# Optimization experiments

Measured on AMD Instinct MI355X. Metric: run time of the kernel, lower is better.

## Reference

```python
import jax, jax.numpy as jnp
import numpy as np
from functools import partial

EPS = 1e-5
CHANS = [(3, 64), (64, 64), (64, 128), (128, 128), (128, 256), (256, 256), (256, 256), (256, 256)]

def conv3d(x, w):
    # x: [B,X,Y,Z,Cin], w: [3,3,3,Cin,Cout]; Minkowski stride-1 conv keeps coords -> SAME padding
    return jax.lax.conv_general_dilated(x, w, window_strides=(1, 1, 1), padding='SAME',
                                        dimension_numbers=('NDHWC', 'DHWIO', 'NDHWC'))

def bn(x, g, b):
    # training-mode batch norm over all voxels (MinkowskiBatchNorm forward)
    m = jnp.mean(x, axis=(0, 1, 2, 3))
    v = jnp.var(x, axis=(0, 1, 2, 3))
    return (x - m) * jax.lax.rsqrt(v + EPS) * g + b

def maxpool2(x):
    return jax.lax.reduce_window(x, -jnp.inf, jax.lax.max,
                                 (1, 2, 2, 2, 1), (1, 2, 2, 2, 1), 'VALID')

def setup_inputs() -> dict:
    key = jax.random.key(0)
    ks = jax.random.split(key, 32)
    inp = {'x': jax.random.normal(ks[0], (2, 64, 64, 64, 3), dtype=jnp.float32)}
    for i, (ci, co) in enumerate(CHANS):
        scale = (2.0 / (27 * ci)) ** 0.5  # kaiming for 3x3x3 conv
        inp[f'w{i+1}'] = jax.random.normal(ks[1 + i], (3, 3, 3, ci, co), dtype=jnp.float32) * scale
        inp[f'g{i+1}'] = jnp.ones((co,), dtype=jnp.float32)
        inp[f'b{i+1}'] = jnp.zeros((co,), dtype=jnp.float32)
    inp['wl'] = jax.random.normal(ks[20], (256, 256), dtype=jnp.float32) * (1.0 / 16.0)
    inp['bl'] = jnp.zeros((256,), dtype=jnp.float32)
    return inp

def reference(x, w1, g1, b1, w2, g2, b2, w3, g3, b3, w4, g4, b4,
              w5, g5, b5, w6, g6, b6, w7, g7, b7, w8, g8, b8, wl, bl):
    h = jax.nn.relu(bn(conv3d(x, w1), g1, b1))
    h = jax.nn.relu(bn(conv3d(h, w2), g2, b2))
    h = maxpool2(h)                                   # 64 -> 32
    h = jax.nn.relu(bn(conv3d(h, w3), g3, b3))
    h = jax.nn.relu(bn(conv3d(h, w4), g4, b4))
    h = maxpool2(h)                                   # 32 -> 16
    h = jax.nn.relu(bn(conv3d(h, w5), g5, b5))
    h = jax.nn.relu(bn(conv3d(h, w6), g6, b6))
    h = jax.nn.relu(bn(conv3d(h, w7), g7, b7))
    h = maxpool2(h)                                   # 16 -> 8
    h = bn(conv3d(h, w8), g8, b8)                     # no ReLU before global pool in source
    h = jnp.mean(h, axis=(1, 2, 3))                   # MinkowskiGlobalPooling (avg over coords)
    return h @ wl + bl                                # MinkowskiLinear(256, out_feat)
```

## Files before the change

### kernel.cpp

```cpp
#include <hip/hip_runtime.h>
#include <stdint.h>


typedef _Float16 f16;
typedef _Float16 f16x8 __attribute__((ext_vector_type(8)));
typedef _Float16 f16x4 __attribute__((ext_vector_type(4)));
typedef float f32x4 __attribute__((ext_vector_type(4)));

__device__ __forceinline__ int xcd_swz(int bx, int nbx) {
  const int q = nbx >> 3, r = nbx & 7;
  const int x = bx & 7, o = bx >> 3;
  return (x < r ? x * (q + 1) : r * (q + 1) + (x - r) * q) + o;
}

struct WArgs {
  const float* src[8];
  int end[8];
  int S[8], G[8], CR[8], CO[8];
};
__global__ __launch_bounds__(256) void wprep_all(WArgs a, f16* __restrict__ wf)
{
  const int e = blockIdx.x * 256 + threadIdx.x;
  int li = 0;
  while (li < 7 && e >= a.end[li]) ++li;
  if (e >= a.end[li]) return;
  const int base = li ? a.end[li - 1] : 0;
  int x = e - base;
  const int i = x & 7;
  const int l = (x >> 3) & 63;
  int r = x >> 9;
  const int g = r % a.G[li]; r /= a.G[li];
  const int s = r % a.S[li]; r /= a.S[li];
  const int t = r;
  const int k = s * 32 + ((l >> 4) << 3) + i;
  const int co = g * 16 + (l & 15);
  float v;
  if (li == 0) {
    const int tap = k >> 3, ci = k & 7;
    v = (ci < 3 && tap < 27) ? a.src[0][((long)tap * 3 + ci) * 64 + co] : 0.f;
  } else {
    v = (k < a.CR[li]) ? a.src[li][((long)t * a.CR[li] + k) * a.CO[li] + co] : 0.f;
  }
  wf[e] = (f16)v;
}

__global__ __launch_bounds__(256) void conv1_mfma(
    const float* __restrict__ xin, const f16* __restrict__ wf,
    f16* __restrict__ out, float* __restrict__ part)
{
  constexpr int Z = 64, Y = 64, X = 64, L = 4;
  constexpr int RB = 48;
  constexpr int SLAB = (L + 2) * (Z + 2) * RB;
  __shared__ __align__(16) char slab[3 * SLAB];
  __shared__ float sstat[4][2][64];

  const int tid = threadIdx.x;
  const int lane = tid & 63;
  const int wr = tid >> 6;

  const int bxs = xcd_swz(blockIdx.x, gridDim.x);
  const long vb = (long)bxs * 256;
  const int n = (int)(vb >> 18);
  const int rem = (int)(vb & 262143);
  const int x0 = rem >> 12;
  const int y0 = (rem >> 6) & 63;

  if (tid < 36) {
    const int s = tid / 12, pr = tid % 12;
    const int row = (pr >> 1) * (Z + 2) + (pr & 1) * (Z + 1);
    const f16x8 hz = {};
    *(f16x8*)(slab + s * SLAB + row * RB) = hz;
  }

  for (int rr2 = tid; rr2 < 3 * (L + 2) * Z; rr2 += 256) {
    const int s = rr2 / ((L + 2) * Z);
    const int rr = rr2 % ((L + 2) * Z);
    const int li = rr / Z, z = rr % Z;
    const int xs = x0 + s - 1, ys = y0 - 1 + li;
    f16x8 h = {};
    if (xs >= 0 && xs < X && ys >= 0 && ys < Y) {
      const float* p = xin + (((long)(n * X + xs) * Y + ys) * Z + z) * 3;
      h[0] = (f16)p[0]; h[1] = (f16)p[1]; h[2] = (f16)p[2];
    }
    *(f16x8*)(slab + s * SLAB + (li * (Z + 2) + 1 + z) * RB) = h;
  }

  int abase[4];
  #pragma unroll
  for (int r = 0; r < 4; ++r) {
    const int vl = wr * 64 + r * 16 + (lane & 15);
    abase[r] = ((vl >> 6) * (Z + 2) + (vl & 63)) * RB;
  }
  const int c = lane >> 4;
  int rofftab[7];
  #pragma unroll
  for (int j = 0; j < 7; ++j) {
    const int tap = 4 * j + c;
    if (tap < 27) {
      const int dx = tap / 9, dy = (tap / 3) % 3, dz = tap % 3;
      rofftab[j] = dx * SLAB + (dy * (Z + 2) + dz) * RB;
    } else {
      rofftab[j] = 0;
    }
  }

  f32x4 acc[4][4];
  const f32x4 fz = {0.f, 0.f, 0.f, 0.f};
  #pragma unroll
  for (int r = 0; r < 4; ++r)
    #pragma unroll
    for (int cc = 0; cc < 4; ++cc) acc[r][cc] = fz;

  __syncthreads();

  #pragma unroll
  for (int j = 0; j < 7; ++j) {
    f16x8 av[4];
    #pragma unroll
    for (int r = 0; r < 4; ++r)
      av[r] = *(const f16x8*)(slab + abase[r] + rofftab[j]);
    f16x8 bv[4];
    #pragma unroll
    for (int c2 = 0; c2 < 4; ++c2)
      bv[c2] = *(const f16x8*)((const char*)wf + ((j * 4 + c2) << 10) + (lane << 4));
    #pragma unroll
    for (int r = 0; r < 4; ++r)
      #pragma unroll
      for (int c2 = 0; c2 < 4; ++c2)
        acc[r][c2] = __builtin_amdgcn_mfma_f32_16x16x32_f16(av[r], bv[c2], acc[r][c2], 0, 0, 0);
  }

  const long vgbase = vb + wr * 64;
  #pragma unroll
  for (int r = 0; r < 4; ++r)
    #pragma unroll
    for (int cc = 0; cc < 4; ++cc)
      #pragma unroll
      for (int q = 0; q < 4; ++q) {
        const long vox = vgbase + r * 16 + ((lane >> 4) << 2) + q;
        const int co = cc * 16 + (lane & 15);
        out[vox * 64 + co] = (f16)acc[r][cc][q];
      }

  float s4[4], q4[4];
  #pragma unroll
  for (int cc = 0; cc < 4; ++cc) {
    float s = 0.f, q = 0.f;
    #pragma unroll
    for (int r = 0; r < 4; ++r)
      #pragma unroll
      for (int qd = 0; qd < 4; ++qd) {
        const float v = acc[r][cc][qd];
        s += v;
        q = fmaf(v, v, q);
      }
    s4[cc] = s; q4[cc] = q;
  }
  #pragma unroll
  for (int cc = 0; cc < 4; ++cc) {
    s4[cc] += __shfl_xor(s4[cc], 16);
    s4[cc] += __shfl_xor(s4[cc], 32);
    q4[cc] += __shfl_xor(q4[cc], 16);
    q4[cc] += __shfl_xor(q4[cc], 32);
  }
  if (lane < 16) {
    #pragma unroll
    for (int cc = 0; cc < 4; ++cc) {
      sstat[wr][0][cc * 16 + lane] = s4[cc];
      sstat[wr][1][cc * 16 + lane] = q4[cc];
    }
  }
  __syncthreads();
  for (int t = tid; t < 128; t += 256) {
    const int k = (t >> 6) & 1, ch = t & 63;
    float v = 0.f;
    #pragma unroll
    for (int w2 = 0; w2 < 4; ++w2) v += sstat[w2][k][ch];
    part[(long)bxs * 128 + k * 64 + ch] = v;
  }
}

__global__ __launch_bounds__(256) void bnpad(
    const f16* __restrict__ in, f16* __restrict__ outp,
    const float* __restrict__ sc, const float* __restrict__ sh)
{
  const long NT = 2L * 66 * 66 * 66 * 8;
  long idx = (long)blockIdx.x * 256 + threadIdx.x;
  if (idx >= NT) return;
  const int c8 = (int)(idx & 7);
  long v = idx >> 3;
  const int zp = (int)(v % 66); v /= 66;
  const int yp = (int)(v % 66); v /= 66;
  const int xp = (int)(v % 66);
  const int n = (int)(v / 66);
  f16x8 h = {};
  if (xp >= 1 && xp <= 64 && yp >= 1 && yp <= 64 && zp >= 1 && zp <= 64) {
    const long src = ((((long)n * 64 + xp - 1) * 64 + yp - 1) * 64 + zp - 1) * 64 + c8 * 8;
    h = *(const f16x8*)(in + src);
    const int ci = c8 * 8;
    const float4 s0 = *(const float4*)(sc + ci);
    const float4 s1 = *(const float4*)(sc + ci + 4);
    const float4 h0 = *(const float4*)(sh + ci);
    const float4 h1 = *(const float4*)(sh + ci + 4);
    h[0] = (f16)fmaxf(fmaf((float)h[0], s0.x, h0.x), 0.f);
    h[1] = (f16)fmaxf(fmaf((float)h[1], s0.y, h0.y), 0.f);
    h[2] = (f16)fmaxf(fmaf((float)h[2], s0.z, h0.z), 0.f);
    h[3] = (f16)fmaxf(fmaf((float)h[3], s0.w, h0.w), 0.f);
    h[4] = (f16)fmaxf(fmaf((float)h[4], s1.x, h1.x), 0.f);
    h[5] = (f16)fmaxf(fmaf((float)h[5], s1.y, h1.y), 0.f);
    h[6] = (f16)fmaxf(fmaf((float)h[6], s1.z, h1.z), 0.f);
    h[7] = (f16)fmaxf(fmaf((float)h[7], s1.w, h1.w), 0.f);
  }
  *(f16x8*)(outp + idx * 8) = h;
}

__global__ __launch_bounds__(256) void conv2_dma(
    const f16* __restrict__ xp, const f16* __restrict__ wf,
    f16* __restrict__ out, float* __restrict__ part)
{
  constexpr int ZP = 66;
  constexpr int RB = 128;
  constexpr int SLABB = 51200;
  __shared__ __align__(1024) char slab[SLABB];
  __shared__ float sstat[4][2][64];

  const int tid = threadIdx.x;
  const int lane = tid & 63;
  const int wv = tid >> 6;

  const int bxs = xcd_swz(blockIdx.x, gridDim.x);
  const long vb = (long)bxs * 256;
  const int n = (int)(vb >> 18);
  const int rem = (int)(vb & 262143);
  const int x0 = rem >> 12;
  const int y0 = (rem >> 6) & 63;

  const int srcoff = ((lane >> 3) << 7) | ((((lane & 7) ^ ((lane >> 3) & 7))) << 4);

  int arow[4];
  #pragma unroll
  for (int r = 0; r < 4; ++r) {
    const int vl = wv * 64 + r * 16 + (lane & 15);
    arow[r] = (vl >> 6) * ZP + (vl & 63);
  }
  const int kbyte = (lane >> 4) << 4;

  f32x4 acc[4][4];
  const f32x4 fz = {0.f, 0.f, 0.f, 0.f};
  #pragma unroll
  for (int r = 0; r < 4; ++r)
    #pragma unroll
    for (int c = 0; c < 4; ++c) acc[r][c] = fz;

  for (int dx = 0; dx < 3; ++dx) {
    __syncthreads();
    const char* gsrc = (const char*)xp +
        (((long)(n * 66 + (x0 + dx)) * 66 + y0) * (long)(ZP * 64 * 2));
    for (int i = wv; i < 50; i += 4) {
      __builtin_amdgcn_global_load_lds(
          (const __attribute__((address_space(1))) uint32_t*)(const void*)(gsrc + (long)i * 1024 + srcoff),
          (__attribute__((address_space(3))) uint32_t*)(void*)(slab + i * 1024),
          16, 0, 0);
    }
    __syncthreads();

    for (int s = 0; s < 2; ++s) {
      #pragma unroll
      for (int dy = 0; dy < 3; ++dy) {
        #pragma unroll
        for (int dzi = 0; dzi < 3; ++dzi) {
          f16x8 av[4];
          #pragma unroll
          for (int r = 0; r < 4; ++r) {
            const int row = arow[r] + dy * ZP + dzi;
            av[r] = *(const f16x8*)(slab + row * RB +
                      ((s * 64 + kbyte) ^ ((row & 7) << 4)));
          }
          const int t = dx * 9 + dy * 3 + dzi;
          f16x8 bv[4];
          #pragma unroll
          for (int c = 0; c < 4; ++c)
            bv[c] = *(const f16x8*)((const char*)wf +
                      (((long)(t * 2 + s) * 4 + c) << 10) + (lane << 4));
          #pragma unroll
          for (int r = 0; r < 4; ++r)
            #pragma unroll
            for (int c = 0; c < 4; ++c)
              acc[r][c] = __builtin_amdgcn_mfma_f32_16x16x32_f16(av[r], bv[c], acc[r][c], 0, 0, 0);
        }
      }
    }
  }

  const long vgbase = vb + wv * 64;
  #pragma unroll
  for (int r = 0; r < 4; ++r)
    #pragma unroll
    for (int c = 0; c < 4; ++c)
      #pragma unroll
      for (int q = 0; q < 4; ++q) {
        const long vox = vgbase + r * 16 + ((lane >> 4) << 2) + q;
        const int co = c * 16 + (lane & 15);
        out[vox * 64 + co] = (f16)acc[r][c][q];
      }

  float s4[4], q4[4];
  #pragma unroll
  for (int c = 0; c < 4; ++c) {
    float s = 0.f, q = 0.f;
    #pragma unroll
    for (int r = 0; r < 4; ++r)
      #pragma unroll
      for (int qd = 0; qd < 4; ++qd) {
        const float v = acc[r][c][qd];
        s += v;
        q = fmaf(v, v, q);
      }
    s4[c] = s; q4[c] = q;
  }
  #pragma unroll
  for (int c = 0; c < 4; ++c) {
    s4[c] += __shfl_xor(s4[c], 16);
    s4[c] += __shfl_xor(s4[c], 32);
    q4[c] += __shfl_xor(q4[c], 16);
    q4[c] += __shfl_xor(q4[c], 32);
  }
  if (lane < 16) {
    #pragma unroll
    for (int c = 0; c < 4; ++c) {
      sstat[wv][0][c * 16 + lane] = s4[c];
      sstat[wv][1][c * 16 + lane] = q4[c];
    }
  }
  __syncthreads();
  for (int t = tid; t < 128; t += 256) {
    const int k = (t >> 6) & 1, ch = t & 63;
    float v = 0.f;
    #pragma unroll
    for (int w2 = 0; w2 < 4; ++w2) v += sstat[w2][k][ch];
    part[(long)bxs * 128 + k * 64 + ch] = v;
  }
}

template<int CIN, int Z, int WR, int WC, bool HASBN, int SS>
__global__ __launch_bounds__(WR*WC*64) void conv_mfma(
    const f16* __restrict__ xin, const f16* __restrict__ wf,
    f16* __restrict__ out, int X, int Y, int Co,
    const float* __restrict__ sc, const float* __restrict__ sh,
    float* __restrict__ part, int partBase,
    float* __restrict__ pout, long outE)
{
  constexpr int NTHR = WR * WC * 64;
  constexpr int L = 64 * WR / Z;
  constexpr int RB = (CIN + 8) * 2;
  constexpr int S = CIN / 32;
  constexpr int COW = 64 * WC;
  constexpr bool SPLIT = (SS > 0);
  __shared__ __align__(16) char slab[(L + 2) * (Z + 2) * RB];
  __shared__ float sstat[SPLIT ? 1 : WR * WC][2][64];

  const int tid = threadIdx.x;
  const int lane = tid & 63;
  const int wv = tid >> 6;
  const int wr = wv / WC, wc = wv % WC;

  const int bxs = xcd_swz(blockIdx.x, gridDim.x);
  const long vb = (long)bxs * (64 * WR);
  const int XYZ = X * Y * Z;
  const int n = (int)(vb / XYZ);
  const int rem = (int)(vb % XYZ);
  const int x0 = rem / (Y * Z);
  const int y0 = (rem % (Y * Z)) / Z;
  const int co0 = blockIdx.y * COW;
  const int Gtot = Co >> 4;
  const int g0 = (co0 >> 4) + wc * 4;

  int abase[4];
  #pragma unroll
  for (int r = 0; r < 4; ++r) {
    const int vl = wr * 64 + r * 16 + (lane & 15);
    abase[r] = ((vl / Z) * (Z + 2) + (vl % Z)) * RB + ((lane >> 4) << 4);
  }

  f32x4 acc[4][4];
  const f32x4 fz = {0.f, 0.f, 0.f, 0.f};
  #pragma unroll
  for (int r = 0; r < 4; ++r)
    #pragma unroll
    for (int c = 0; c < 4; ++c) acc[r][c] = fz;

  {
    const f16x8 hz = {};
    for (int e = tid * 8; e < (L + 2) * 2 * CIN; e += NTHR * 8) {
      const int pr = e / CIN, ci = e % CIN;
      const int row = (pr >> 1) * (Z + 2) + (pr & 1) * (Z + 1);
      *(f16x8*)(slab + row * RB + ci * 2) = hz;
    }
  }

  auto stage = [&](int dx) {
    const int xs = x0 + dx - 1;
    const bool xok = (xs >= 0) && (xs < X);
    const long gv0 = ((long)(n * X + xs) * Y + (y0 - 1)) * Z;
    constexpr int NE = (L + 2) * Z * CIN;
    for (int e = tid * 8; e < NE; e += NTHR * 8) {
      const int rr = e / CIN, ci = e % CIN;
      const int li = rr / Z, z = rr % Z;
      const int ys = y0 - 1 + li;
      f16x8 h = {};
      if (xok && ys >= 0 && ys < Y) {
        h = *(const f16x8*)(xin + (gv0 + rr) * CIN + ci);
        if constexpr (HASBN) {
          const float4 s0 = *(const float4*)(sc + ci);
          const float4 s1 = *(const float4*)(sc + ci + 4);
          const float4 h0 = *(const float4*)(sh + ci);
          const float4 h1 = *(const float4*)(sh + ci + 4);
          h[0] = (f16)fmaxf(fmaf((float)h[0], s0.x, h0.x), 0.f);
          h[1] = (f16)fmaxf(fmaf((float)h[1], s0.y, h0.y), 0.f);
          h[2] = (f16)fmaxf(fmaf((float)h[2], s0.z, h0.z), 0.f);
          h[3] = (f16)fmaxf(fmaf((float)h[3], s0.w, h0.w), 0.f);
          h[4] = (f16)fmaxf(fmaf((float)h[4], s1.x, h1.x), 0.f);
          h[5] = (f16)fmaxf(fmaf((float)h[5], s1.y, h1.y), 0.f);
          h[6] = (f16)fmaxf(fmaf((float)h[6], s1.z, h1.z), 0.f);
          h[7] = (f16)fmaxf(fmaf((float)h[7], s1.w, h1.w), 0.f);
        }
      }
      *(f16x8*)(slab + (li * (Z + 2) + 1 + z) * RB + ci * 2) = h;
    }
  };

  auto ktaps = [&](int dx, int s) {
    #pragma unroll
    for (int dy = 0; dy < 3; ++dy) {
      #pragma unroll
      for (int dzi = 0; dzi < 3; ++dzi) {
        f16x8 av[4];
        #pragma unroll
        for (int r = 0; r < 4; ++r)
          av[r] = *(const f16x8*)(slab + abase[r] + s * 64 + (dy * (Z + 2) + dzi) * RB);
        const int t = dx * 9 + dy * 3 + dzi;
        f16x8 bv[4];
        #pragma unroll
        for (int c = 0; c < 4; ++c)
          bv[c] = *(const f16x8*)((const char*)wf +
                    (((long)(t * S + s) * Gtot + g0 + c) << 10) + (lane << 4));
        #pragma unroll
        for (int r = 0; r < 4; ++r)
          #pragma unroll
          for (int c = 0; c < 4; ++c)
            acc[r][c] = __builtin_amdgcn_mfma_f32_16x16x32_f16(av[r], bv[c], acc[r][c], 0, 0, 0);
      }
    }
  };

  if constexpr (SPLIT) {
    constexpr int SCH = S / SS;
    const int zb = blockIdx.z;
    const int dx = zb / SS;
    const int s0 = (zb % SS) * SCH;
    stage(dx);
    __syncthreads();
    #pragma unroll
    for (int si = 0; si < SCH; ++si) ktaps(dx, s0 + si);
  } else {
    for (int dx = 0; dx < 3; ++dx) {
      __syncthreads();
      stage(dx);
      __syncthreads();
      for (int s = 0; s < S; ++s) ktaps(dx, s);
    }
  }

  const long vgbase = vb + wr * 64;
  const int cobase = co0 + wc * 64;
  if constexpr (SPLIT) {
    float* pb = pout + (long)blockIdx.z * outE;
    #pragma unroll
    for (int r = 0; r < 4; ++r)
      #pragma unroll
      for (int c = 0; c < 4; ++c)
        #pragma unroll
        for (int q = 0; q < 4; ++q) {
          const long vox = vgbase + r * 16 + ((lane >> 4) << 2) + q;
          const int co = cobase + c * 16 + (lane & 15);
          pb[vox * Co + co] = acc[r][c][q];
        }
    return;
  }

  #pragma unroll
  for (int r = 0; r < 4; ++r)
    #pragma unroll
    for (int c = 0; c < 4; ++c)
      #pragma unroll
      for (int q = 0; q < 4; ++q) {
        const long vox = vgbase + r * 16 + ((lane >> 4) << 2) + q;
        const int co = cobase + c * 16 + (lane & 15);
        out[vox * Co + co] = (f16)acc[r][c][q];
      }

  float s4[4], q4[4];
  #pragma unroll
  for (int c = 0; c < 4; ++c) {
    float s = 0.f, q = 0.f;
    #pragma unroll
    for (int r = 0; r < 4; ++r)
      #pragma unroll
      for (int qd = 0; qd < 4; ++qd) {
        const float v = acc[r][c][qd];
        s += v;
        q = fmaf(v, v, q);
      }
    s4[c] = s; q4[c] = q;
  }
  #pragma unroll
  for (int c = 0; c < 4; ++c) {
    s4[c] += __shfl_xor(s4[c], 16);
    s4[c] += __shfl_xor(s4[c], 32);
    q4[c] += __shfl_xor(q4[c], 16);
    q4[c] += __shfl_xor(q4[c], 32);
  }
  if (lane < 16) {
    #pragma unroll
    for (int c = 0; c < 4; ++c) {
      sstat[wv][0][c * 16 + lane] = s4[c];
      sstat[wv][1][c * 16 + lane] = q4[c];
    }
  }
  __syncthreads();
  const long entry = (long)blockIdx.y * gridDim.x + bxs + partBase;
  for (int t = tid; t < WC * 128; t += NTHR) {
    const int wcc = t >> 7, k = (t >> 6) & 1, ch = t & 63;
    float v = 0.f;
    #pragma unroll
    for (int wr2 = 0; wr2 < WR; ++wr2) v += sstat[wr2 * WC + wcc][k][ch];
    part[entry * (2 * COW) + k * COW + wcc * 64 + ch] = v;
  }
}

__global__ __launch_bounds__(256) void reduce_stats(
    const float* __restrict__ pout, f16* __restrict__ out,
    long outE, int KS, int vpb, float* __restrict__ part)
{
  const int tid = threadIdx.x;
  const int wv = tid >> 6, lane = tid & 63;
  const int vbase = blockIdx.x * vpb;
  float4 s = {0.f, 0.f, 0.f, 0.f}, q = {0.f, 0.f, 0.f, 0.f};
  for (int v = vbase + wv; v < vbase + vpb; v += 4) {
    const long e = (long)v * 256 + lane * 4;
    float4 o = *(const float4*)(pout + e);
    for (int z = 1; z < KS; ++z) {
      const float4 p = *(const float4*)(pout + (long)z * outE + e);
      o.x += p.x; o.y += p.y; o.z += p.z; o.w += p.w;
    }
    f16x4 ov = {(f16)o.x, (f16)o.y, (f16)o.z, (f16)o.w};
    *(f16x4*)(out + e) = ov;
    s.x += o.x; s.y += o.y; s.z += o.z; s.w += o.w;
    q.x = fmaf(o.x, o.x, q.x); q.y = fmaf(o.y, o.y, q.y);
    q.z = fmaf(o.z, o.z, q.z); q.w = fmaf(o.w, o.w, q.w);
  }
  __shared__ float st[4][2][256];
  *(float4*)&st[wv][0][lane * 4] = s;
  *(float4*)&st[wv][1][lane * 4] = q;
  __syncthreads();
  for (int t = tid; t < 512; t += 256) {
    const int k = t >> 8, ch = t & 255;
    part[(long)blockIdx.x * 512 + k * 256 + ch] =
        st[0][k][ch] + st[1][k][ch] + st[2][k][ch] + st[3][k][ch];
  }
}

__global__ __launch_bounds__(256) void stats_final(
    const float* __restrict__ part, int nbx, int CoWin, long nvox,
    const float* __restrict__ g, const float* __restrict__ b,
    float* __restrict__ sc, float* __restrict__ sh)
{
  const int c = blockIdx.x;
  const int by = c / CoWin;
  const int cw = c % CoWin;
  const int tid = threadIdx.x;
  float s = 0.f, ss = 0.f;
  for (int i = tid; i < nbx; i += 256) {
    const long base = ((long)by * nbx + i) * 2 * CoWin;
    s += part[base + cw];
    ss += part[base + CoWin + cw];
  }
  __shared__ float r0[256];
  __shared__ float r1[256];
  r0[tid] = s; r1[tid] = ss;
  __syncthreads();
  #pragma unroll
  for (int o = 128; o > 0; o >>= 1) {
    if (tid < o) { r0[tid] += r0[tid + o]; r1[tid] += r1[tid + o]; }
    __syncthreads();
  }
  if (tid == 0) {
    const float inv = 1.f / (float)nvox;
    const float m = r0[0] * inv;
    const float var = r1[0] * inv - m * m;
    const float scale = rsqrtf(var + 1e-5f) * g[c];
    sc[c] = scale;
    sh[c] = b[c] - m * scale;
  }
}

__global__ __launch_bounds__(256) void maxpool2_aff(
    const f16* __restrict__ in, f16* __restrict__ out,
    int N, int X, int Y, int Z, int C,
    const float* __restrict__ sc, const float* __restrict__ sh)
{
  const int OX = X >> 1, OY = Y >> 1, OZ = Z >> 1;
  const int c4n = C >> 2;
  const long nout = (long)N * OX * OY * OZ * c4n;
  long idx = (long)blockIdx.x * 256 + threadIdx.x;
  if (idx >= nout) return;
  const int c4 = (int)(idx % c4n);
  long v = idx / c4n;
  const int oz = (int)(v % OZ); v /= OZ;
  const int oy = (int)(v % OY); v /= OY;
  const int ox = (int)(v % OX);
  const int n = (int)(v / OX);
  const long sx = (long)Y * Z * C, sy = (long)Z * C, sz = C;
  const long base = ((((long)n * X + 2 * ox) * Y + 2 * oy) * Z + 2 * oz) * (long)C + 4L * c4;
  f16x4 m = *(const f16x4*)(in + base);
  #pragma unroll
  for (int dd = 1; dd < 8; ++dd) {
    const int dxp = dd >> 2, dyp = (dd >> 1) & 1, dzp = dd & 1;
    const f16x4 t = *(const f16x4*)(in + base + dxp * sx + dyp * sy + dzp * sz);
    #pragma unroll
    for (int i = 0; i < 4; ++i) m[i] = (t[i] > m[i]) ? t[i] : m[i];
  }
  const int c = 4 * c4;
  const float4 s4 = *(const float4*)(sc + c);
  const float4 h4 = *(const float4*)(sh + c);
  f16x4 r;
  r[0] = (f16)fmaxf(fmaf((float)m[0], s4.x, h4.x), 0.f);
  r[1] = (f16)fmaxf(fmaf((float)m[1], s4.y, h4.y), 0.f);
  r[2] = (f16)fmaxf(fmaf((float)m[2], s4.z, h4.z), 0.f);
  r[3] = (f16)fmaxf(fmaf((float)m[3], s4.w, h4.w), 0.f);
  *(f16x4*)(out + idx * 4) = r;
}

__global__ __launch_bounds__(256) void head_mean(
    const f16* __restrict__ x8, const float* __restrict__ sc, const float* __restrict__ sh,
    float* __restrict__ hbuf)
{
  const int n = blockIdx.x, cg = blockIdx.y;
  const int tx = threadIdx.x & 63, ty = threadIdx.x >> 6;
  const int c = cg * 64 + tx;
  float s = 0.f;
  for (int v = ty; v < 512; v += 4) s += (float)x8[((long)n * 512 + v) * 256 + c];
  __shared__ float red[4][64];
  red[ty][tx] = s;
  __syncthreads();
  if (ty == 0) {
    s = red[0][tx] + red[1][tx] + red[2][tx] + red[3][tx];
    hbuf[n * 256 + c] = fmaf(s * (1.f / 512.f), sc[c], sh[c]);
  }
}

__global__ __launch_bounds__(256) void head_mv(
    const float* __restrict__ hbuf, const float* __restrict__ wl,
    const float* __restrict__ bl, float* __restrict__ out)
{
  const int n = blockIdx.x, og = blockIdx.y;
  const int tx = threadIdx.x & 63, ty = threadIdx.x >> 6;
  const int oc = og * 64 + tx;
  float a = 0.f;
  const int k0 = ty * 64;
  for (int k = k0; k < k0 + 64; ++k)
    a = fmaf(hbuf[n * 256 + k], wl[(long)k * 256 + oc], a);
  __shared__ float red[4][64];
  red[ty][tx] = a;
  __syncthreads();
  if (ty == 0)
    out[n * 256 + oc] = red[0][tx] + red[1][tx] + red[2][tx] + red[3][tx] + bl[oc];
}

extern "C" void kernel_launch(void* const* d_in, const int* in_sizes, int n_in,
                              void* d_out, int out_size, void* d_ws, size_t ws_size,
                              hipStream_t stream)
{
  const float* x = (const float*)d_in[0];
  const float* W[8];
  const float* G[8];
  const float* B[8];
  for (int i = 0; i < 8; ++i) {
    W[i] = (const float*)d_in[1 + 3 * i];
    G[i] = (const float*)d_in[2 + 3 * i];
    B[i] = (const float*)d_in[3 + 3 * i];
  }
  const float* wl = (const float*)d_in[25];
  const float* bl = (const float*)d_in[26];

  char* ws = (char*)d_ws;
  f16*   A    = (f16*)ws;
  f16*   Bb   = (f16*)(ws + (64L << 20));
  f16*   P1   = (f16*)(ws + (128L << 20));
  float* pK   = (float*)(ws + (128L << 20));
  float* part = (float*)(ws + (204L << 20));
  float* scb  = part + 262144L;
  float* shb  = scb + 2048L;
  float* hbuf = shb + 2048L;
  f16*   wfb  = (f16*)(hbuf + 512L);

  const int wfS[8]  = {7, 2, 2, 4, 4, 8, 8, 8};
  const int wfG[8]  = {4, 4, 8, 8, 16, 16, 16, 16};
  const int wfT[8]  = {1, 27, 27, 27, 27, 27, 27, 27};
  const int wfCR[8] = {3, 64, 64, 128, 128, 256, 256, 256};
  const int wfCO[8] = {64, 64, 128, 128, 256, 256, 256, 256};
  long wfOff[9];
  wfOff[0] = 0;
  for (int i = 0; i < 8; ++i) wfOff[i + 1] = wfOff[i] + (long)wfT[i] * wfS[i] * wfG[i] * 512;
  if (ws_size < (size_t)((char*)(wfb + wfOff[8]) - ws)) return;
  auto WF = [&](int i) { return wfb + wfOff[i]; };
  auto SC = [&](int i) { return scb + i * 256; };
  auto SH = [&](int i) { return shb + i * 256; };

  {
    WArgs a;
    for (int i = 0; i < 8; ++i) {
      a.src[i] = W[i]; a.end[i] = (int)wfOff[i + 1];
      a.S[i] = wfS[i]; a.G[i] = wfG[i]; a.CR[i] = wfCR[i]; a.CO[i] = wfCO[i];
    }
    wprep_all<<<(unsigned)((wfOff[8] + 255) / 256), 256, 0, stream>>>(a, wfb);
  }

  auto fin = [&](int layer, int nbx, int CoWin, int C, long nvox) {
    stats_final<<<C, 256, 0, stream>>>(part, nbx, CoWin, nvox,
                                       G[layer], B[layer], SC(layer), SH(layer));
  };
  auto pool_aff = [&](const f16* in, f16* ob, int N, int Xd, int Yd, int Zd, int C, int layer) {
    const long nout = (long)N * (Xd / 2) * (Yd / 2) * (Zd / 2) * (C / 4);
    maxpool2_aff<<<(unsigned)((nout + 255) / 256), 256, 0, stream>>>(
        in, ob, N, Xd, Yd, Zd, C, SC(layer), SH(layer));
  };

  conv1_mfma<<<2048, 256, 0, stream>>>(x, WF(0), A, part);
  fin(0, 2048, 64, 64, 524288);
  {
    const long NT = 2L * 66 * 66 * 66 * 8;
    bnpad<<<(unsigned)((NT + 255) / 256), 256, 0, stream>>>(A, P1, SC(0), SH(0));
  }
  conv2_dma<<<2048, 256, 0, stream>>>(P1, WF(1), Bb, part);
  fin(1, 2048, 64, 64, 524288);
  pool_aff(Bb, A, 2, 64, 64, 64, 64, 1);

  conv_mfma<64, 32, 2, 2, false, 0><<<dim3(512, 1), 256, 0, stream>>>(
      A, WF(2), Bb, 32, 32, 128, nullptr, nullptr, part, 0, nullptr, 0);
  fin(2, 512, 128, 128, 65536);
  conv_mfma<128, 32, 2, 2, true, 0><<<dim3(512, 1), 256, 0, stream>>>(
      Bb, WF(3), A, 32, 32, 128, SC(2), SH(2), part, 0, nullptr, 0);
  fin(3, 512, 128, 128, 65536);
  pool_aff(A, Bb, 2, 32, 32, 32, 128, 3);

  const long E16 = 2097152;
  conv_mfma<128, 16, 1, 4, false, 1><<<dim3(128, 1, 3), 256, 0, stream>>>(
      Bb, WF(4), nullptr, 16, 16, 256, nullptr, nullptr, nullptr, 0, pK, E16);
  reduce_stats<<<256, 256, 0, stream>>>(pK, A, E16, 3, 32, part);
  fin(4, 256, 256, 256, 8192);
  conv_mfma<256, 16, 1, 4, true, 1><<<dim3(128, 1, 3), 256, 0, stream>>>(
      A, WF(5), nullptr, 16, 16, 256, SC(4), SH(4), nullptr, 0, pK, E16);
  reduce_stats<<<256, 256, 0, stream>>>(pK, Bb, E16, 3, 32, part);
  fin(5, 256, 256, 256, 8192);
  conv_mfma<256, 16, 1, 4, true, 1><<<dim3(128, 1, 3), 256, 0, stream>>>(
      Bb, WF(6), nullptr, 16, 16, 256, SC(5), SH(5), nullptr, 0, pK, E16);
  reduce_stats<<<256, 256, 0, stream>>>(pK, A, E16, 3, 32, part);
  fin(6, 256, 256, 256, 8192);
  pool_aff(A, Bb, 2, 16, 16, 16, 256, 6);

  const long E8 = 262144;
  conv_mfma<256, 8, 1, 4, false, 4><<<dim3(16, 1, 12), 256, 0, stream>>>(
      Bb, WF(7), nullptr, 8, 8, 256, nullptr, nullptr, nullptr, 0, pK, E8);
  reduce_stats<<<256, 256, 0, stream>>>(pK, A, E8, 12, 4, part);
  fin(7, 256, 256, 256, 1024);

  head_mean<<<dim3(2, 4), 256, 0, stream>>>(A, SC(7), SH(7), hbuf);
  head_mv<<<dim3(2, 4), 256, 0, stream>>>(hbuf, wl, bl, (float*)d_out);
}
```

Measured before the change: 578.4 us.

## Fuse BN+ReLU+padding into conv2 by staging all three x-slabs in LDS

Removes the separate bnpad kernel that wrote a padded, normalized copy of the layer-1 output. conv2 now loads the unpadded layer-1 activations directly, applies the batch-norm affine and ReLU in registers, and writes all three dx slabs plus zeroed halo rows into LDS before computing. This saves one full read-write pass over the activation tensor and a kernel launch. In exchange it gives up the asynchronous global-to-LDS DMA loads, uses about 152KB of LDS per block, which cuts occupancy, and adds ALU work during staging.

```diff
diff --git a/kernel.cpp b/kernel.cpp
--- a/kernel.cpp
+++ b/kernel.cpp
@@ -1,5 +1,4 @@
 #include <hip/hip_runtime.h>
-#include <stdint.h>
 
 
 typedef _Float16 f16;
@@ -180,48 +179,16 @@
   }
 }
 
-__global__ __launch_bounds__(256) void bnpad(
-    const f16* __restrict__ in, f16* __restrict__ outp,
-    const float* __restrict__ sc, const float* __restrict__ sh)
-{
-  const long NT = 2L * 66 * 66 * 66 * 8;
-  long idx = (long)blockIdx.x * 256 + threadIdx.x;
-  if (idx >= NT) return;
-  const int c8 = (int)(idx & 7);
-  long v = idx >> 3;
-  const int zp = (int)(v % 66); v /= 66;
-  const int yp = (int)(v % 66); v /= 66;
-  const int xp = (int)(v % 66);
-  const int n = (int)(v / 66);
-  f16x8 h = {};
-  if (xp >= 1 && xp <= 64 && yp >= 1 && yp <= 64 && zp >= 1 && zp <= 64) {
-    const long src = ((((long)n * 64 + xp - 1) * 64 + yp - 1) * 64 + zp - 1) * 64 + c8 * 8;
-    h = *(const f16x8*)(in + src);
-    const int ci = c8 * 8;
-    const float4 s0 = *(const float4*)(sc + ci);
-    const float4 s1 = *(const float4*)(sc + ci + 4);
-    const float4 h0 = *(const float4*)(sh + ci);
-    const float4 h1 = *(const float4*)(sh + ci + 4);
-    h[0] = (f16)fmaxf(fmaf((float)h[0], s0.x, h0.x), 0.f);
-    h[1] = (f16)fmaxf(fmaf((float)h[1], s0.y, h0.y), 0.f);
-    h[2] = (f16)fmaxf(fmaf((float)h[2], s0.z, h0.z), 0.f);
-    h[3] = (f16)fmaxf(fmaf((float)h[3], s0.w, h0.w), 0.f);
-    h[4] = (f16)fmaxf(fmaf((float)h[4], s1.x, h1.x), 0.f);
-    h[5] = (f16)fmaxf(fmaf((float)h[5], s1.y, h1.y), 0.f);
-    h[6] = (f16)fmaxf(fmaf((float)h[6], s1.z, h1.z), 0.f);
-    h[7] = (f16)fmaxf(fmaf((float)h[7], s1.w, h1.w), 0.f);
-  }
-  *(f16x8*)(outp + idx * 8) = h;
-}
-
-__global__ __launch_bounds__(256) void conv2_dma(
-    const f16* __restrict__ xp, const f16* __restrict__ wf,
-    f16* __restrict__ out, float* __restrict__ part)
-{
-  constexpr int ZP = 66;
+__global__ __launch_bounds__(256) void conv2_res3(
+    const f16* __restrict__ xin, const f16* __restrict__ wf,
+    f16* __restrict__ out,
+    const float* __restrict__ sc, const float* __restrict__ sh,
+    float* __restrict__ part)
+{
+  constexpr int Z = 64, Y = 64, X = 64;
   constexpr int RB = 128;
-  constexpr int SLABB = 51200;
-  __shared__ __align__(1024) char slab[SLABB];
+  constexpr int SLAB = 6 * (Z + 2) * RB;
+  __shared__ __align__(16) char slab[3 * SLAB];
   __shared__ float sstat[4][2][64];
 
   const int tid = threadIdx.x;
@@ -235,13 +202,51 @@
   const int x0 = rem >> 12;
   const int y0 = (rem >> 6) & 63;
 
-  const int srcoff = ((lane >> 3) << 7) | ((((lane & 7) ^ ((lane >> 3) & 7))) << 4);
+  {
+    const f16x8 hz = {};
+    for (int e = tid; e < 288; e += 256) {
+      const int c8 = e & 7;
+      const int r = e >> 3;
+      const int pr = r % 12, s = r / 12;
+      const int row = (pr >> 1) * (Z + 2) + (pr & 1) * (Z + 1);
+      *(f16x8*)(slab + s * SLAB + row * RB + (((c8 * 16)) ^ ((row & 7) << 4))) = hz;
+    }
+  }
+
+  for (int dx = 0; dx < 3; ++dx) {
+    const int xs = x0 + dx - 1;
+    const bool xok = (xs >= 0) && (xs < X);
+    const long gv0 = ((long)(n * X + xs) * Y + (y0 - 1)) * Z;
+    for (int e = tid * 8; e < 6 * Z * 64; e += 2048) {
+      const int rr = e >> 6, ci = e & 63;
+      const int li = rr >> 6, z = rr & 63;
+      const int ys = y0 - 1 + li;
+      f16x8 h = {};
+      if (xok && ys >= 0 && ys < Y) {
+        h = *(const f16x8*)(xin + (gv0 + rr) * 64 + ci);
+        const float4 s0 = *(const float4*)(sc + ci);
+        const float4 s1 = *(const float4*)(sc + ci + 4);
+        const float4 h0 = *(const float4*)(sh + ci);
+        const float4 h1 = *(const float4*)(sh + ci + 4);
+        h[0] = (f16)fmaxf(fmaf((float)h[0], s0.x, h0.x), 0.f);
+        h[1] = (f16)fmaxf(fmaf((float)h[1], s0.y, h0.y), 0.f);
+        h[2] = (f16)fmaxf(fmaf((float)h[2], s0.z, h0.z), 0.f);
+        h[3] = (f16)fmaxf(fmaf((float)h[3], s0.w, h0.w), 0.f);
+        h[4] = (f16)fmaxf(fmaf((float)h[4], s1.x, h1.x), 0.f);
+        h[5] = (f16)fmaxf(fmaf((float)h[5], s1.y, h1.y), 0.f);
+        h[6] = (f16)fmaxf(fmaf((float)h[6], s1.z, h1.z), 0.f);
+        h[7] = (f16)fmaxf(fmaf((float)h[7], s1.w, h1.w), 0.f);
+      }
+      const int row = li * (Z + 2) + 1 + z;
+      *(f16x8*)(slab + dx * SLAB + row * RB + ((ci * 2) ^ ((row & 7) << 4))) = h;
+    }
+  }
 
   int arow[4];
   #pragma unroll
   for (int r = 0; r < 4; ++r) {
     const int vl = wv * 64 + r * 16 + (lane & 15);
-    arow[r] = (vl >> 6) * ZP + (vl & 63);
+    arow[r] = (vl >> 6) * (Z + 2) + (vl & 63);
   }
   const int kbyte = (lane >> 4) << 4;
 
@@ -252,18 +257,10 @@
     #pragma unroll
     for (int c = 0; c < 4; ++c) acc[r][c] = fz;
 
+  __syncthreads();
+
   for (int dx = 0; dx < 3; ++dx) {
-    __syncthreads();
-    const char* gsrc = (const char*)xp +
-        (((long)(n * 66 + (x0 + dx)) * 66 + y0) * (long)(ZP * 64 * 2));
-    for (int i = wv; i < 50; i += 4) {
-      __builtin_amdgcn_global_load_lds(
-          (const __attribute__((address_space(1))) uint32_t*)(const void*)(gsrc + (long)i * 1024 + srcoff),
-          (__attribute__((address_space(3))) uint32_t*)(void*)(slab + i * 1024),
-          16, 0, 0);
-    }
-    __syncthreads();
-
+    const char* sl = slab + dx * SLAB;
     for (int s = 0; s < 2; ++s) {
       #pragma unroll
       for (int dy = 0; dy < 3; ++dy) {
@@ -272,8 +269,8 @@
           f16x8 av[4];
           #pragma unroll
           for (int r = 0; r < 4; ++r) {
-            const int row = arow[r] + dy * ZP + dzi;
-            av[r] = *(const f16x8*)(slab + row * RB +
+            const int row = arow[r] + dy * (Z + 2) + dzi;
+            av[r] = *(const f16x8*)(sl + row * RB +
                       ((s * 64 + kbyte) ^ ((row & 7) << 4)));
           }
           const int t = dx * 9 + dy * 3 + dzi;
@@ -696,9 +693,8 @@
   char* ws = (char*)d_ws;
   f16*   A    = (f16*)ws;
   f16*   Bb   = (f16*)(ws + (64L << 20));
-  f16*   P1   = (f16*)(ws + (128L << 20));
   float* pK   = (float*)(ws + (128L << 20));
-  float* part = (float*)(ws + (204L << 20));
+  float* part = (float*)(ws + (152L << 20));
   float* scb  = part + 262144L;
   float* shb  = scb + 2048L;
   float* hbuf = shb + 2048L;
@@ -738,11 +734,7 @@
 
   conv1_mfma<<<2048, 256, 0, stream>>>(x, WF(0), A, part);
   fin(0, 2048, 64, 64, 524288);
-  {
-    const long NT = 2L * 66 * 66 * 66 * 8;
-    bnpad<<<(unsigned)((NT + 255) / 256), 256, 0, stream>>>(A, P1, SC(0), SH(0));
-  }
-  conv2_dma<<<2048, 256, 0, stream>>>(P1, WF(1), Bb, part);
+  conv2_res3<<<2048, 256, 0, stream>>>(A, WF(1), Bb, SC(0), SH(0), part);
   fin(1, 2048, 64, 64, 524288);
   pool_aff(Bb, A, 2, 64, 64, 64, 64, 1);
 
```

After: 635.3 us. 9.8% more time.
